# Kernel tuning notes

Measured on AMD Instinct MI355X. Metric: run time of the kernel, lower is better.

## Reference

```python
import jax, jax.numpy as jnp
import numpy as np
import math

INPUT_DIM = 1024
QUERY_DIM = 1024
VALUE_DIM = 1024

def setup_inputs() -> dict:
    key = jax.random.key(0)
    ks = jax.random.split(key, 7)
    N, T, D = 4, 4096, INPUT_DIM
    s_in = 1.0 / math.sqrt(D)
    X = jax.random.normal(ks[0], (N, T, D), dtype=jnp.float32)
    # torch.nn.Linear weights: (out, in), init ~ U(-1/sqrt(in), 1/sqrt(in))
    Wq = jax.random.uniform(ks[1], (QUERY_DIM, D), jnp.float32, -s_in, s_in)
    bq = jax.random.uniform(ks[2], (QUERY_DIM,), jnp.float32, -s_in, s_in)
    Wk = jax.random.uniform(ks[3], (QUERY_DIM, D), jnp.float32, -s_in, s_in)
    bk = jax.random.uniform(ks[4], (QUERY_DIM,), jnp.float32, -s_in, s_in)
    Wv = jax.random.uniform(ks[5], (VALUE_DIM, D), jnp.float32, -s_in, s_in)
    bv = jax.random.uniform(ks[6], (VALUE_DIM,), jnp.float32, -s_in, s_in)
    return {"X": X, "Wq": Wq, "bq": bq, "Wk": Wk, "bk": bk, "Wv": Wv, "bv": bv}

def reference(X, Wq, bq, Wk, bk, Wv, bv):
    N, T, D = X.shape
    q = jnp.einsum('ntd,qd->ntq', X, Wq) + bq  # (N,T,Q)
    k = jnp.einsum('ntd,qd->ntq', X, Wk) + bk  # (N,T,Q)
    v = jnp.einsum('ntd,vd->ntv', X, Wv) + bv  # (N,T,V)
    # NOTE: original scales by sqrt(D) = sqrt(input_dim), not sqrt(query_dim)
    scores = jnp.einsum('ntq,nsq->nts', q, k) / jnp.sqrt(jnp.asarray(D, X.dtype))
    attn = jax.nn.softmax(scores, axis=-1)  # (N,T,T)
    return jnp.einsum('nts,nsv->ntv', attn, v)
```

## Files before the change

kernel.cpp:

```cpp
#include <hip/hip_runtime.h>
#include <stdint.h>

typedef unsigned short u16;
typedef unsigned char u8;
typedef unsigned int u32;
typedef short shortx8 __attribute__((ext_vector_type(8)));
typedef float floatx4 __attribute__((ext_vector_type(4)));
typedef int intx4 __attribute__((ext_vector_type(4)));
typedef int intx8 __attribute__((ext_vector_type(8)));

__device__ __forceinline__ u16 f2bf(float f) {
    u32 u = __builtin_bit_cast(u32, f);
    u = (u + 0x7fffu + ((u >> 16) & 1u)) >> 16;
    return (u16)u;
}

#if defined(__has_builtin)
#  if __has_builtin(__builtin_amdgcn_cvt_pk_fp8_f32)
#    define HAVE_CVT_FP8 1
#  endif
#  if __has_builtin(__builtin_amdgcn_global_load_lds)
#    define HAVE_GLL 1
#  endif
#endif
#ifndef HAVE_CVT_FP8
#  define HAVE_CVT_FP8 0
#endif
#ifndef HAVE_GLL
#  define HAVE_GLL 0
#endif

__device__ __forceinline__ u8 f2fp8(float f) {
#if HAVE_CVT_FP8
    return (u8)(__builtin_amdgcn_cvt_pk_fp8_f32(f, f, 0, false) & 0xff);
#else
    u32 u = __builtin_bit_cast(u32, f);
    u32 s = (u >> 24) & 0x80u;
    u32 m = u & 0x7fffffffu;
    if (m >= 0x43e00000u) return (u8)(s | 0x7eu);
    if (m < 0x3c800000u) {
        int q = __float2int_rn(__builtin_bit_cast(float, m) * 512.f);
        return (u8)(s | (u32)q);
    }
    u32 r = m + 0x7ffffu + ((m >> 20) & 1u);
    u32 code = (((r >> 23) - 120u) << 3) | ((r >> 20) & 7u);
    if (code > 0x7eu) code = 0x7eu;
    return (u8)(s | code);
#endif
}

#if HAVE_GLL
__device__ __forceinline__ void gload_lds16(const void* g, void* l) {
    __builtin_amdgcn_global_load_lds(
        (const __attribute__((address_space(1))) u32*)g,
        (__attribute__((address_space(3))) u32*)l,
        16, 0, 0);
}
#endif

template <typename OutT, int MODE, int SWZ>
__global__ __launch_bounds__(256, 2) void gemm_bt(
    const u16* __restrict__ Ag, const u16* __restrict__ Bg, OutT* __restrict__ Cg,
    int lda, int ldb, int ldc, int K,
    const float* __restrict__ aux, float scale,
    long long sAz, long long sBz, long long sCz, long long sXz,
    int swz_nhalf)
{
    __shared__ u16 smem[4][128 * 32];

    int z, mb, nb;
    if constexpr (SWZ) {
        const int f = blockIdx.x, xcd = f & 7, g = f >> 3;
        z = xcd >> 1;
        mb = g & 31;
        nb = (xcd & 1) * swz_nhalf + (g >> 5);
    } else {
        z = blockIdx.z; mb = blockIdx.y; nb = blockIdx.x;
    }
    const int m0 = mb * 128, n0 = nb * 128;

    const u16* A = Ag + (long long)z * sAz;
    const u16* B = Bg + (long long)z * sBz;
    OutT* C = Cg + (long long)z * sCz;
    const float* auxp = aux ? aux + (long long)z * sXz : nullptr;

    const int tid = threadIdx.x, lane = tid & 63, wv = tid >> 6;

    const int srow = lane >> 2;
    const int schunk = (lane & 3) * 8;
    const u16* gA0 = A + (size_t)(m0 + wv * 16 + srow) * lda + schunk;
    const u16* gA1 = gA0 + (size_t)64 * lda;
    const u16* gB0 = B + (size_t)(n0 + wv * 16 + srow) * ldb + schunk;
    const u16* gB1 = gB0 + (size_t)64 * ldb;
    const int wb = wv * 512;

    const int wm = (wv & 1) * 64, wn = (wv >> 1) * 64;
    const int mi = lane & 15, kq = lane >> 4;

    floatx4 acc[4][4] = {};

    for (int k0 = 0; k0 < K; k0 += 64) {
#if HAVE_GLL
        gload_lds16(gA0,      &smem[0][wb]);
        gload_lds16(gA1,      &smem[0][2048 + wb]);
        gload_lds16(gA0 + 32, &smem[1][wb]);
        gload_lds16(gA1 + 32, &smem[1][2048 + wb]);
        gload_lds16(gB0,      &smem[2][wb]);
        gload_lds16(gB1,      &smem[2][2048 + wb]);
        gload_lds16(gB0 + 32, &smem[3][wb]);
        gload_lds16(gB1 + 32, &smem[3][2048 + wb]);
#else
        *(shortx8*)(&smem[0][wb] + lane * 8)        = *(const shortx8*)gA0;
        *(shortx8*)(&smem[0][2048 + wb] + lane * 8) = *(const shortx8*)gA1;
        *(shortx8*)(&smem[1][wb] + lane * 8)        = *(const shortx8*)(gA0 + 32);
        *(shortx8*)(&smem[1][2048 + wb] + lane * 8) = *(const shortx8*)(gA1 + 32);
        *(shortx8*)(&smem[2][wb] + lane * 8)        = *(const shortx8*)gB0;
        *(shortx8*)(&smem[2][2048 + wb] + lane * 8) = *(const shortx8*)gB1;
        *(shortx8*)(&smem[3][wb] + lane * 8)        = *(const shortx8*)(gB0 + 32);
        *(shortx8*)(&smem[3][2048 + wb] + lane * 8) = *(const shortx8*)(gB1 + 32);
#endif
        gA0 += 64; gA1 += 64; gB0 += 64; gB1 += 64;
        __syncthreads();

#pragma unroll
        for (int h = 0; h < 2; h++) {
            const u16* Ap = smem[h];
            const u16* Bp = smem[2 + h];
            shortx8 af[4], bfr[4];
#pragma unroll
            for (int i = 0; i < 4; i++)
                af[i] = *(const shortx8*)(Ap + (wm + i * 16 + mi) * 32 + kq * 8);
#pragma unroll
            for (int j = 0; j < 4; j++)
                bfr[j] = *(const shortx8*)(Bp + (wn + j * 16 + mi) * 32 + kq * 8);
#pragma unroll
            for (int i = 0; i < 4; i++)
#pragma unroll
                for (int j = 0; j < 4; j++)
                    acc[i][j] = __builtin_amdgcn_mfma_f32_16x16x32_bf16(
                        af[i], bfr[j], acc[i][j], 0, 0, 0);
        }
        __syncthreads();
    }

    float cb[4];
    if constexpr (MODE == 1) {
#pragma unroll
        for (int j = 0; j < 4; j++) cb[j] = auxp[n0 + wn + j * 16 + mi];
    }

    if constexpr (sizeof(OutT) == 2) {
        u16* ct = &smem[0][0];
#pragma unroll
        for (int i = 0; i < 4; i++) {
#pragma unroll
            for (int r = 0; r < 4; r++) {
                const int lrow = wm + i * 16 + kq * 4 + r;
                float radd = 0.f;
                if constexpr (MODE == 2) radd = auxp[m0 + lrow];
#pragma unroll
                for (int j = 0; j < 4; j++) {
                    float v = acc[i][j][r];
                    if constexpr (MODE == 1) v += cb[j];
                    if constexpr (MODE == 2) v += radd;
                    ct[lrow * 128 + wn + j * 16 + mi] = f2bf(v);
                }
            }
        }
        __syncthreads();
#pragma unroll
        for (int it = 0; it < 8; it++) {
            const int fl = (it * 256 + tid) * 8;
            const int row = fl >> 7, col = fl & 127;
            *(uint4*)(C + (size_t)(m0 + row) * ldc + n0 + col) =
                *(const uint4*)(ct + fl);
        }
    } else if constexpr (sizeof(OutT) == 1) {
        u8* ct = (u8*)&smem[0][0];
#pragma unroll
        for (int i = 0; i < 4; i++) {
#pragma unroll
            for (int r = 0; r < 4; r++) {
                const int lrow = wm + i * 16 + kq * 4 + r;
#pragma unroll
                for (int j = 0; j < 4; j++) {
                    float v = acc[i][j][r];
                    if constexpr (MODE == 1) v += cb[j];
                    ct[lrow * 128 + wn + j * 16 + mi] = f2fp8(v);
                }
            }
        }
        __syncthreads();
        u8* base = (u8*)Cg + ((size_t)mb * 16 + nb) * 16384;
#pragma unroll
        for (int it = 0; it < 4; it++) {
            const int fl = (it * 256 + tid) * 16;
            const int row = fl >> 7, c = (fl >> 4) & 7;
            *(uint4*)(base + row * 128 + ((c ^ (row & 7)) << 4)) =
                *(const uint4*)(ct + fl);
        }
    } else {
#pragma unroll
        for (int i = 0; i < 4; i++) {
#pragma unroll
            for (int r = 0; r < 4; r++) {
                const int row = m0 + wm + i * 16 + kq * 4 + r;
                float rmul = 1.f;
                if constexpr (MODE == 4) rmul = 1.0f / auxp[row];
                OutT* crow = C + (size_t)row * ldc;
#pragma unroll
                for (int j = 0; j < 4; j++) {
                    const int col = n0 + wn + j * 16 + mi;
                    crow[col] = acc[i][j][r] * rmul;
                }
            }
        }
    }
}

__device__ __forceinline__ intx8 cat8(intx4 a, intx4 b) {
    return __builtin_shufflevector(a, b, 0, 1, 2, 3, 4, 5, 6, 7);
}

template <int SWZ>
__global__ __launch_bounds__(256, 1) void gemm_fp8_scores(
    const u8* __restrict__ QKt, u16* __restrict__ Pg,
    float* __restrict__ sums, float scale, int T)
{
    __shared__ u8 smem[4][16384];

    int z, mb, nb;
    if constexpr (SWZ) {
        const int f = blockIdx.x, xcd = f & 7, g = f >> 3;
        z = xcd >> 1;
        const int s = g >> 7, t = g & 127;
        mb = (s << 3) | (t & 7);
        nb = (xcd & 1) * 16 + (t >> 3);
    } else {
        z = blockIdx.z; mb = blockIdx.y; nb = blockIdx.x;
    }
    const int m0 = mb * 128, n0 = nb * 128;

    const u8* At = QKt + ((size_t)(z * 32 + mb) * 16) * 16384;
    const u8* Bt = QKt + ((size_t)(z * 32 + nb) * 16 + 8) * 16384;
    u16* P = Pg + (size_t)z * T * T;
    float* sumz = sums + (size_t)z * T;

    const int tid = threadIdx.x, lane = tid & 63, wv = tid >> 6;
    const int wm = (wv & 1) * 64, wn = (wv >> 1) * 64;
    const int mi = lane & 15, kq = lane >> 4;
    const int xm = mi & 7;
    const int off0 = ((2 * kq) ^ xm) * 16;
    const int off1 = ((2 * kq + 1) ^ xm) * 16;

    const u8* gA = At + wv * 4096 + lane * 16;
    const u8* gB = Bt + wv * 4096 + lane * 16;

    floatx4 acc[4][4] = {};

#if HAVE_GLL
#pragma unroll
    for (int i = 0; i < 4; i++) {
        gload_lds16(gA + i * 1024, &smem[0][wv * 4096] + i * 1024);
        gload_lds16(gB + i * 1024, &smem[1][wv * 4096] + i * 1024);
    }
#else
#pragma unroll
    for (int i = 0; i < 4; i++) {
        *(uint4*)(&smem[0][wv * 4096] + i * 1024 + lane * 16) = *(const uint4*)(gA + i * 1024);
        *(uint4*)(&smem[1][wv * 4096] + i * 1024 + lane * 16) = *(const uint4*)(gB + i * 1024);
    }
#endif
    gA += 16384; gB += 16384;
    __syncthreads();

    int cur = 0;
    for (int kp = 0; kp < 8; kp++) {
        const int nxt = cur ^ 2;
        if (kp < 7) {
#if HAVE_GLL
#pragma unroll
            for (int i = 0; i < 4; i++) {
                gload_lds16(gA + i * 1024, &smem[nxt][wv * 4096] + i * 1024);
                gload_lds16(gB + i * 1024, &smem[nxt + 1][wv * 4096] + i * 1024);
            }
#else
#pragma unroll
            for (int i = 0; i < 4; i++) {
                *(uint4*)(&smem[nxt][wv * 4096] + i * 1024 + lane * 16) = *(const uint4*)(gA + i * 1024);
                *(uint4*)(&smem[nxt + 1][wv * 4096] + i * 1024 + lane * 16) = *(const uint4*)(gB + i * 1024);
            }
#endif
            gA += 16384; gB += 16384;
        }
        __builtin_amdgcn_sched_barrier(0);

        const u8* Ap = &smem[cur][0];
        const u8* Bp = &smem[cur + 1][0];
        intx8 af[4];
#pragma unroll
        for (int i = 0; i < 4; i++) {
            const u8* p = Ap + (wm + i * 16 + mi) * 128;
            af[i] = cat8(*(const intx4*)(p + off0), *(const intx4*)(p + off1));
        }
#pragma unroll
        for (int j = 0; j < 4; j++) {
            const u8* p = Bp + (wn + j * 16 + mi) * 128;
            const intx8 bfr = cat8(*(const intx4*)(p + off0), *(const intx4*)(p + off1));
#pragma unroll
            for (int i = 0; i < 4; i++)
                acc[i][j] = __builtin_amdgcn_mfma_scale_f32_16x16x128_f8f6f4(
                    af[i], bfr, acc[i][j], 0, 0,
                    0, 0x7f7f7f7f, 0, 0x7f7f7f7f);
        }
        __syncthreads();
        cur = nxt;
    }

    u16* ct = (u16*)&smem[0][0];
#pragma unroll
    for (int i = 0; i < 4; i++) {
#pragma unroll
        for (int r = 0; r < 4; r++) {
            const int lrow = wm + i * 16 + kq * 4 + r;
            float rs = 0.f;
#pragma unroll
            for (int j = 0; j < 4; j++) {
                float v = __expf(acc[i][j][r] * scale);
                rs += v;
                ct[lrow * 128 + wn + j * 16 + mi] = f2bf(v);
            }
            rs += __shfl_xor(rs, 1);
            rs += __shfl_xor(rs, 2);
            rs += __shfl_xor(rs, 4);
            rs += __shfl_xor(rs, 8);
            if (mi == 0) atomicAdd(&sumz[m0 + lrow], rs);
        }
    }
    __syncthreads();
#pragma unroll
    for (int it = 0; it < 8; it++) {
        const int fl = (it * 256 + tid) * 8;
        const int row = fl >> 7, col = fl & 127;
        *(uint4*)(P + (size_t)(m0 + row) * T + n0 + col) = *(const uint4*)(ct + fl);
    }
}

__global__ __launch_bounds__(256) void cvt_bf16(const float* __restrict__ s,
                                                u16* __restrict__ d, int n8)
{
    int i = blockIdx.x * 256 + threadIdx.x;
    if (i >= n8) return;
    const float4* sp = (const float4*)s;
    float4 a = sp[2 * i], b = sp[2 * i + 1];
    uint4 o;
    o.x = (u32)f2bf(a.x) | ((u32)f2bf(a.y) << 16);
    o.y = (u32)f2bf(a.z) | ((u32)f2bf(a.w) << 16);
    o.z = (u32)f2bf(b.x) | ((u32)f2bf(b.y) << 16);
    o.w = (u32)f2bf(b.z) | ((u32)f2bf(b.w) << 16);
    *(uint4*)(d + 8 * i) = o;
}

__global__ void concat2(const float* __restrict__ a, const float* __restrict__ b,
                        float* __restrict__ d, int n)
{
    int i = blockIdx.x * 256 + threadIdx.x;
    if (i < n) d[i] = a[i];
    else if (i < 2 * n) d[i] = b[i - n];
}

extern "C" void kernel_launch(void* const* d_in, const int* in_sizes, int n_in,
                              void* d_out, int out_size, void* d_ws, size_t ws_size,
                              hipStream_t stream)
{
    const float* X  = (const float*)d_in[0];
    const float* Wq = (const float*)d_in[1];
    const float* bq = (const float*)d_in[2];
    const float* Wk = (const float*)d_in[3];
    const float* bk = (const float*)d_in[4];
    const float* Wv = (const float*)d_in[5];
    const float* bv = (const float*)d_in[6];
    float* out = (float*)d_out;

    const int T = 4096, NT = 4 * T;
    const long long TL = T;

    char* ws = (char*)d_ws;
    size_t off = 0;
    auto alloc = [&](size_t bytes) {
        char* p = ws + off;
        off += (bytes + 255) & ~(size_t)255;
        return p;
    };
    u16*   Wqk  = (u16*)alloc((size_t)2048 * 1024 * 2);
    u16*   Wvb  = (u16*)alloc((size_t)1024 * 1024 * 2);
    float* bqk  = (float*)alloc(2048 * 4);
    u8*    QKt  = (u8*)alloc((size_t)128 * 16 * 16384);
    u16*   Vt   = (u16*)alloc((size_t)1024 * NT * 2);
    float* sums = (float*)alloc((size_t)NT * 4);
    size_t pbase = off;
    u16*   Xb   = (u16*)alloc((size_t)NT * 1024 * 2);
    u16*   P    = Xb;

    const size_t need_batched = pbase + (size_t)4 * T * T * 2;
    const bool batched = ws_size >= need_batched;

    cvt_bf16<<<dim3((NT * 1024 / 8 + 255) / 256), dim3(256), 0, stream>>>(X, Xb, NT * 1024 / 8);
    cvt_bf16<<<dim3(512), dim3(256), 0, stream>>>(Wq, Wqk, 1024 * 1024 / 8);
    cvt_bf16<<<dim3(512), dim3(256), 0, stream>>>(Wk, Wqk + 1024 * 1024, 1024 * 1024 / 8);
    cvt_bf16<<<dim3(512), dim3(256), 0, stream>>>(Wv, Wvb, 1024 * 1024 / 8);
    concat2<<<dim3(8), dim3(256), 0, stream>>>(bq, bk, bqk, 1024);
    hipMemsetAsync(sums, 0, (size_t)NT * 4, stream);

    gemm_bt<u8, 1, 0><<<dim3(16, 128, 1), dim3(256), 0, stream>>>(
        Xb, Wqk, QKt, 1024, 1024, 0, 1024, bqk, 0.f, 0, 0, 0, 0, 0);

    gemm_bt<u16, 2, 0><<<dim3(128, 8, 1), dim3(256), 0, stream>>>(
        Wvb, Xb, Vt, 1024, 1024, NT, 1024, bv, 0.f, 0, 0, 0, 0, 0);

    if (batched) {
        gemm_fp8_scores<1><<<dim3(4096), dim3(256), 0, stream>>>(
            QKt, P, sums, 0.03125f, T);
        gemm_bt<float, 4, 1><<<dim3(1024), dim3(256), 0, stream>>>(
            P, Vt, out, T, NT, 1024, T, sums, 0.f,
            TL * T, TL, TL * 1024, TL, 4);
    } else {
        for (int z = 0; z < 4; z++) {
            gemm_fp8_scores<0><<<dim3(32, 32, 1), dim3(256), 0, stream>>>(
                QKt + (size_t)z * 32 * 16 * 16384, P, sums + (size_t)z * T, 0.03125f, T);
            gemm_bt<float, 4, 0><<<dim3(8, 32, 1), dim3(256), 0, stream>>>(
                P, Vt + (size_t)z * T, out + (size_t)z * T * 1024,
                T, NT, 1024, T, sums + (size_t)z * T, 0.f, 0, 0, 0, 0, 0);
        }
    }
    (void)in_sizes; (void)n_in; (void)out_size;
}
```

Before: 535.1 us.

## Add 256x256-tile 512-thread PV GEMM kernel replacing generic batched gemm_bt

```diff
diff --git a/kernel.cpp b/kernel.cpp
--- a/kernel.cpp
+++ b/kernel.cpp
@@ -218,6 +218,117 @@
     }
 }
 
+__global__ __launch_bounds__(512, 2) void gemm_pv256(
+    const u16* __restrict__ Pg, const u16* __restrict__ Vt,
+    float* __restrict__ outg, const float* __restrict__ sums, int T, int NT)
+{
+    __shared__ u8 smem[2][65536];
+
+    const int f = blockIdx.x, xcd = f & 7, g = f >> 3;
+    const int z = xcd >> 1;
+    const int nb = (xcd & 1) * 2 + (g >> 4);
+    const int mb = g & 15;
+    const int m0 = mb * 256, n0 = nb * 256;
+
+    const u8* Pz = (const u8*)(Pg + (size_t)z * T * T);
+    const u8* Vz = (const u8*)(Vt + (size_t)z * T);
+    const float* sumz = sums + (size_t)z * T;
+
+    const int tid = threadIdx.x, lane = tid & 63, wv = tid >> 6;
+    const int wr = wv >> 2, wc = wv & 3;
+    const int mi = lane & 15, kq = lane >> 4;
+
+    const int srow = lane >> 3;
+    const int schunk = ((lane & 7) ^ srow) << 4;
+    const size_t ldPb = (size_t)T * 2, ldVb = (size_t)NT * 2;
+    const u8* gsrc;
+    size_t grstride;
+    int lds_r0;
+    if (wv < 4) {
+        gsrc = Pz + (size_t)(m0 + wv * 64 + srow) * ldPb + schunk;
+        grstride = ldPb * 8;
+        lds_r0 = wv * 8192;
+    } else {
+        gsrc = Vz + (size_t)(n0 + (wv - 4) * 64 + srow) * ldVb + schunk;
+        grstride = ldVb * 8;
+        lds_r0 = 32768 + (wv - 4) * 8192;
+    }
+
+    const int csw0 = ((0 * 4 + kq) ^ (mi & 7)) << 4;
+    const int csw1 = ((1 * 4 + kq) ^ (mi & 7)) << 4;
+
+    floatx4 acc[8][4] = {};
+
+    auto stage = [&](int slot, int kt) {
+        const u8* s0 = gsrc + (size_t)kt * 128;
+        u8* l0 = &smem[slot][lds_r0];
+#if HAVE_GLL
+#pragma unroll
+        for (int q = 0; q < 8; q++)
+            gload_lds16(s0 + (size_t)q * grstride, l0 + q * 1024);
+#else
+#pragma unroll
+        for (int q = 0; q < 8; q++)
+            *(uint4*)(l0 + q * 1024 + lane * 16) =
+                *(const uint4*)(s0 + (size_t)q * grstride);
+#endif
+    };
+
+    stage(0, 0);
+    __syncthreads();
+
+    for (int kt = 0; kt < 64; kt++) {
+        const int s = kt & 1;
+        if (kt < 63) stage(s ^ 1, kt + 1);
+        __builtin_amdgcn_sched_barrier(0);
+
+        const u8* Ab = &smem[s][0];
+        const u8* Bb = &smem[s][32768];
+
+        shortx8 bfr[4][2];
+#pragma unroll
+        for (int nj = 0; nj < 4; nj++) {
+            const u8* p = Bb + (wc * 64 + nj * 16 + mi) * 128;
+            bfr[nj][0] = *(const shortx8*)(p + csw0);
+            bfr[nj][1] = *(const shortx8*)(p + csw1);
+        }
+#pragma unroll
+        for (int mh = 0; mh < 2; mh++) {
+            shortx8 af[4][2];
+#pragma unroll
+            for (int fi = 0; fi < 4; fi++) {
+                const u8* p = Ab + (wr * 128 + (mh * 4 + fi) * 16 + mi) * 128;
+                af[fi][0] = *(const shortx8*)(p + csw0);
+                af[fi][1] = *(const shortx8*)(p + csw1);
+            }
+            __builtin_amdgcn_s_setprio(1);
+#pragma unroll
+            for (int ks = 0; ks < 2; ks++)
+#pragma unroll
+                for (int fi = 0; fi < 4; fi++)
+#pragma unroll
+                    for (int nj = 0; nj < 4; nj++)
+                        acc[mh * 4 + fi][nj] = __builtin_amdgcn_mfma_f32_16x16x32_bf16(
+                            af[fi][ks], bfr[nj][ks], acc[mh * 4 + fi][nj], 0, 0, 0);
+            __builtin_amdgcn_s_setprio(0);
+        }
+        __syncthreads();
+    }
+
+#pragma unroll
+    for (int fr = 0; fr < 8; fr++) {
+#pragma unroll
+        for (int r = 0; r < 4; r++) {
+            const int row = m0 + wr * 128 + fr * 16 + kq * 4 + r;
+            const float rmul = 1.0f / sumz[row];
+            float* crow = outg + ((size_t)z * T + row) * 1024 + n0 + wc * 64 + mi;
+#pragma unroll
+            for (int nj = 0; nj < 4; nj++)
+                crow[nj * 16] = acc[fr][nj][r] * rmul;
+        }
+    }
+}
+
 __device__ __forceinline__ intx8 cat8(intx4 a, intx4 b) {
     return __builtin_shufflevector(a, b, 0, 1, 2, 3, 4, 5, 6, 7);
 }
@@ -295,12 +406,11 @@
         }
         __builtin_amdgcn_sched_barrier(0);
 
-        const u8* Ap = &smem[cur][0];
         const u8* Bp = &smem[cur + 1][0];
         intx8 af[4];
 #pragma unroll
         for (int i = 0; i < 4; i++) {
-            const u8* p = Ap + (wm + i * 16 + mi) * 128;
+            const u8* p = &smem[cur][(wm + i * 16 + mi) * 128];
             af[i] = cat8(*(const intx4*)(p + off0), *(const intx4*)(p + off1));
         }
 #pragma unroll
@@ -421,9 +531,8 @@
     if (batched) {
         gemm_fp8_scores<1><<<dim3(4096), dim3(256), 0, stream>>>(
             QKt, P, sums, 0.03125f, T);
-        gemm_bt<float, 4, 1><<<dim3(1024), dim3(256), 0, stream>>>(
-            P, Vt, out, T, NT, 1024, T, sums, 0.f,
-            TL * T, TL, TL * 1024, TL, 4);
+        gemm_pv256<<<dim3(256), dim3(512), 0, stream>>>(
+            P, Vt, out, sums, T, NT);
     } else {
         for (int z = 0; z < 4; z++) {
             gemm_fp8_scores<0><<<dim3(32, 32, 1), dim3(256), 0, stream>>>(
```

After: 509.5 us. 1.05x faster.
